# Kernel tuning notes

Measured on AMD Instinct MI355X. Metric: run time of the kernel, lower is better.

## Reference

```python
import jax, jax.numpy as jnp
import numpy as np


def setup_inputs() -> dict:
    key = jax.random.key(0)
    ks = jax.random.split(key, 5)
    T, B, C, H, K = 2048, 8, 1024, 16, 7
    s = 1.0 / np.sqrt(C)
    return {
        "x": jax.random.normal(ks[0], (T, B, C), dtype=jnp.float32),
        "w_weight": jax.random.normal(ks[1], (H * K, C), dtype=jnp.float32) * s,
        "glu_w": jax.random.normal(ks[2], (2 * H, C), dtype=jnp.float32) * s,
        "glu_b": jnp.zeros((2 * H,), dtype=jnp.float32),
        "out_w": jax.random.normal(ks[3], (C, C), dtype=jnp.float32) * s,
        "out_b": jnp.zeros((C,), dtype=jnp.float32),
        "padding_l": 6,
    }


def reference(x, w_weight, glu_w, glu_b, out_w, out_b, padding_l):
    # x: (T, B, C) in TBC format
    T, B, C = x.shape
    H = glu_w.shape[0] // 2
    K = w_weight.shape[0] // H
    R = C // H  # channels per head

    # GLU gate: C -> 2H, split last dim, a * sigmoid(b)  -> (T, B, H)
    g = (x @ glu_w.T + glu_b).reshape(T, B, H, 2)
    gate = g[..., 0] * jax.nn.sigmoid(g[..., 1])

    # per-position per-head kernel weights, softmax over K -> (T, B, H, K)
    w = jax.nn.softmax((x @ w_weight.T).reshape(T, B, H, K), axis=-1)

    # depthwise dynamic conv: out[t] = sum_k w[t,k] * x_pad[t + k]
    xh = x.reshape(T, B, H, R)
    xp = jnp.pad(xh, ((padding_l, K - 1 - padding_l), (0, 0), (0, 0), (0, 0)))
    conv = jnp.zeros_like(xh)
    for k in range(K):  # K is small & static; avoids (B,H,T,K,R) unfold blowup
        conv = conv + w[..., k:k + 1] * jax.lax.dynamic_slice_in_dim(xp, k, T, axis=0)

    # gate per head, merge heads, output projection
    out = (conv * gate[..., None]).reshape(T, B, C)
    return out @ out_w.T + out_b
```

## Files before the change

### kernel.cpp

```cpp
#include <hip/hip_runtime.h>
#include <hip/hip_bf16.h>
#include <stdint.h>

#define T_DIM 2048
#define B_DIM 8
#define C_DIM 1024
#define H_DIM 16
#define K_DIM 7
#define M_DIM (T_DIM * B_DIM)
#define NLOG 144
#define CW_STRIDE 128

typedef __attribute__((ext_vector_type(8))) short short8;
typedef __attribute__((ext_vector_type(4))) float floatx4;

__device__ __forceinline__ ushort f2bf(float f) {
    __hip_bfloat16 h = __float2bfloat16(f);
    return *(ushort*)&h;
}

#define S_W  ((size_t)112 * C_DIM)
#define S_G  ((size_t)32 * C_DIM)
#define S_O  ((size_t)C_DIM * C_DIM)
#define S_WG (S_W + S_G)
#define S_CVT (S_WG + S_O)

__global__ __launch_bounds__(256) void cvt_w_kernel(
    const float* __restrict__ w_weight, const float* __restrict__ glu_w,
    const float* __restrict__ out_w,
    ushort* __restrict__ wb, ushort* __restrict__ Wb)
{
    size_t gid = ((size_t)blockIdx.x * 256 + threadIdx.x) * 4;
    const float* src; ushort* dst; size_t off;
    if (gid < S_W)            { src = w_weight; dst = wb;       off = gid; }
    else if (gid < S_WG)      { src = glu_w;    dst = wb + S_W; off = gid - S_W; }
    else                      { src = out_w;    dst = Wb;       off = gid - S_WG; }
    float4 v = *(const float4*)(src + off);
    ushort4 o; o.x = f2bf(v.x); o.y = f2bf(v.y); o.z = f2bf(v.z); o.w = f2bf(v.w);
    *(ushort4*)(dst + off) = o;
}

__global__ __launch_bounds__(256) void logits_kernel(
    const float* __restrict__ x,
    const ushort* __restrict__ wb,
    const float* __restrict__ glu_b,
    float* __restrict__ cw)
{
    __shared__ __align__(16) ushort Bs[2][144 * 32];
    __shared__ float lsm[64][NLOG];

    const int tid = threadIdx.x;
    const int wave = tid >> 6, lane = tid & 63;
    const int fr = lane & 15, q = lane >> 4;
    const int m0 = blockIdx.x * 64;
    const int mrow = m0 + wave * 16 + fr;

    floatx4 acc[9];
#pragma unroll
    for (int j = 0; j < 9; ++j) acc[j] = (floatx4){0.f, 0.f, 0.f, 0.f};

    const float* arow = x + (size_t)mrow * C_DIM + q * 8;

    for (int i = tid; i < 576; i += 256) {
        int r = i >> 2, ch = i & 3;
        __builtin_amdgcn_global_load_lds(
            (const __attribute__((address_space(1))) void*)(wb + (size_t)r * C_DIM + ch * 8),
            (__attribute__((address_space(3))) void*)(&Bs[0][0] + i * 8), 16, 0, 0);
    }
    float4 a0 = *(const float4*)(arow);
    float4 a1 = *(const float4*)(arow + 4);
    __syncthreads();

    for (int kc = 0; kc < 32; ++kc) {
        const int buf = kc & 1;
        if (kc < 31) {
            const ushort* wsrc = wb + (kc + 1) * 32;
            for (int i = tid; i < 576; i += 256) {
                int r = i >> 2, ch = i & 3;
                __builtin_amdgcn_global_load_lds(
                    (const __attribute__((address_space(1))) void*)(wsrc + (size_t)r * C_DIM + ch * 8),
                    (__attribute__((address_space(3))) void*)(&Bs[buf ^ 1][0] + i * 8), 16, 0, 0);
            }
        }
        short8 a;
        a[0] = (short)f2bf(a0.x); a[1] = (short)f2bf(a0.y);
        a[2] = (short)f2bf(a0.z); a[3] = (short)f2bf(a0.w);
        a[4] = (short)f2bf(a1.x); a[5] = (short)f2bf(a1.y);
        a[6] = (short)f2bf(a1.z); a[7] = (short)f2bf(a1.w);
        if (kc < 31) {
            a0 = *(const float4*)(arow + (kc + 1) * 32);
            a1 = *(const float4*)(arow + (kc + 1) * 32 + 4);
        }
#pragma unroll
        for (int j = 0; j < 9; ++j) {
            short8 b = *(const short8*)(&Bs[buf][0] + ((j * 16 + fr) * 4 + q) * 8);
            acc[j] = __builtin_amdgcn_mfma_f32_16x16x32_bf16(a, b, acc[j], 0, 0, 0);
        }
        __syncthreads();
    }

#pragma unroll
    for (int j = 0; j < 9; ++j)
#pragma unroll
        for (int r = 0; r < 4; ++r)
            lsm[wave * 16 + q * 4 + r][j * 16 + fr] = acc[j][r];
    __syncthreads();

    {
        const int row = tid >> 2;
        const int hbase = (tid & 3) * 4;
        float* crow = cw + (size_t)(m0 + row) * CW_STRIDE;
#pragma unroll
        for (int hh = 0; hh < 4; ++hh) {
            const int h = hbase + hh;
            float l[K_DIM];
            float mx = -1e30f;
#pragma unroll
            for (int k = 0; k < K_DIM; ++k) { l[k] = lsm[row][h * K_DIM + k]; mx = fmaxf(mx, l[k]); }
            float s = 0.f;
#pragma unroll
            for (int k = 0; k < K_DIM; ++k) { l[k] = __expf(l[k] - mx); s += l[k]; }
            float inv = 1.f / s;
#pragma unroll
            for (int k = 0; k < K_DIM; ++k) crow[h * K_DIM + k] = l[k] * inv;
            float ga = lsm[row][112 + 2 * h] + glu_b[2 * h];
            float gb = lsm[row][113 + 2 * h] + glu_b[2 * h + 1];
            crow[112 + h] = ga * (1.f / (1.f + __expf(-gb)));
        }
    }
}

__global__ __launch_bounds__(256) void conv_kernel(
    const float* __restrict__ x,
    const float* __restrict__ cw,
    const int* __restrict__ padding_l_,
    ushort* __restrict__ y)
{
    const int lb = (blockIdx.x & 7) * 512 + (blockIdx.x >> 3);
    const int wave = threadIdx.x >> 6, lane = threadIdx.x & 63;
    const int m = lb * 4 + wave;
    const int t = m >> 3;
    const int pad = *padding_l_;
    const int h = lane >> 2;

    const float* crow = cw + (size_t)m * CW_STRIDE;
    float wt[K_DIM];
#pragma unroll
    for (int k = 0; k < K_DIM; ++k) wt[k] = crow[h * K_DIM + k];
    const float g = crow[112 + h];

    const int c0 = lane * 16;
    float av[16];
#pragma unroll
    for (int i = 0; i < 16; ++i) av[i] = 0.f;

#pragma unroll
    for (int k = 0; k < K_DIM; ++k) {
        int ts = t + k - pad;
        if (ts < 0 || ts >= T_DIM) continue;
        float wv = wt[k];
        const float4* xp = (const float4*)(x + ((size_t)m + 8 * (k - pad)) * C_DIM + c0);
        float4 u0 = xp[0], u1 = xp[1], u2 = xp[2], u3 = xp[3];
        av[0]  += wv * u0.x; av[1]  += wv * u0.y; av[2]  += wv * u0.z; av[3]  += wv * u0.w;
        av[4]  += wv * u1.x; av[5]  += wv * u1.y; av[6]  += wv * u1.z; av[7]  += wv * u1.w;
        av[8]  += wv * u2.x; av[9]  += wv * u2.y; av[10] += wv * u2.z; av[11] += wv * u2.w;
        av[12] += wv * u3.x; av[13] += wv * u3.y; av[14] += wv * u3.z; av[15] += wv * u3.w;
    }

    uint32_t o[8];
#pragma unroll
    for (int i = 0; i < 8; ++i)
        o[i] = (uint32_t)f2bf(av[2 * i] * g) | ((uint32_t)f2bf(av[2 * i + 1] * g) << 16);
    uint4* yr = (uint4*)(y + (size_t)m * C_DIM + c0);
    yr[0] = (uint4){o[0], o[1], o[2], o[3]};
    yr[1] = (uint4){o[4], o[5], o[6], o[7]};
}

__global__ __launch_bounds__(256) void out_gemm(
    const ushort* __restrict__ y,
    const ushort* __restrict__ Wb,
    const float* __restrict__ bias,
    float* __restrict__ out)
{
    __shared__ __align__(16) ushort As[128 * 64];
    __shared__ __align__(16) ushort Bs[128 * 64];

    const int bn = blockIdx.x & 7;
    const int bm = blockIdx.x >> 3;
    const int m0 = bm * 128, n0 = bn * 128;
    const int tid = threadIdx.x;
    const int lane = tid & 63, wave = tid >> 6;
    const int wm = (wave >> 1) * 64, wn = (wave & 1) * 64;
    const int fr = lane & 15, q = lane >> 4;

    floatx4 acc[4][4];
#pragma unroll
    for (int i = 0; i < 4; ++i)
#pragma unroll
        for (int j = 0; j < 4; ++j) acc[i][j] = (floatx4){0.f, 0.f, 0.f, 0.f};

    for (int k0 = 0; k0 < C_DIM; k0 += 64) {
        __syncthreads();
#pragma unroll
        for (int j = 0; j < 4; ++j) {
            int idx = j * 256 + tid;
            int r = idx >> 3, cl = idx & 7;
            int ch = cl ^ (r & 7);
            const ushort* ga = y + (size_t)(m0 + r) * C_DIM + k0 + ch * 8;
            __builtin_amdgcn_global_load_lds(
                (const __attribute__((address_space(1))) void*)ga,
                (__attribute__((address_space(3))) void*)(As + idx * 8), 16, 0, 0);
            const ushort* gb = Wb + (size_t)(n0 + r) * C_DIM + k0 + ch * 8;
            __builtin_amdgcn_global_load_lds(
                (const __attribute__((address_space(1))) void*)gb,
                (__attribute__((address_space(3))) void*)(Bs + idx * 8), 16, 0, 0);
        }
        __syncthreads();

#pragma unroll
        for (int s = 0; s < 64; s += 32) {
            const int cbase = (s >> 3) + q;
            short8 a[4], b[4];
#pragma unroll
            for (int i = 0; i < 4; ++i) {
                int r = wm + i * 16 + fr;
                a[i] = *(const short8*)(As + r * 64 + ((cbase ^ (r & 7)) * 8));
            }
#pragma unroll
            for (int j = 0; j < 4; ++j) {
                int r = wn + j * 16 + fr;
                b[j] = *(const short8*)(Bs + r * 64 + ((cbase ^ (r & 7)) * 8));
            }
#pragma unroll
            for (int i = 0; i < 4; ++i)
#pragma unroll
                for (int j = 0; j < 4; ++j)
                    acc[i][j] = __builtin_amdgcn_mfma_f32_16x16x32_bf16(a[i], b[j], acc[i][j], 0, 0, 0);
        }
    }

#pragma unroll
    for (int j = 0; j < 4; ++j) {
        int n = n0 + wn + j * 16 + fr;
        float bv = bias[n];
#pragma unroll
        for (int i = 0; i < 4; ++i) {
#pragma unroll
            for (int r = 0; r < 4; ++r) {
                int m = m0 + wm + i * 16 + q * 4 + r;
                out[(size_t)m * C_DIM + n] = acc[i][j][r] + bv;
            }
        }
    }
}

extern "C" void kernel_launch(void* const* d_in, const int* in_sizes, int n_in,
                              void* d_out, int out_size, void* d_ws, size_t ws_size,
                              hipStream_t stream) {
    const float* x        = (const float*)d_in[0];
    const float* w_weight = (const float*)d_in[1];
    const float* glu_w    = (const float*)d_in[2];
    const float* glu_b    = (const float*)d_in[3];
    const float* out_w    = (const float*)d_in[4];
    const float* out_b    = (const float*)d_in[5];
    const int* padding_l  = (const int*)d_in[6];
    float* out = (float*)d_out;

    char* ws = (char*)d_ws;
    ushort* y  = (ushort*)ws;
    ushort* wb = y + (size_t)M_DIM * C_DIM;
    ushort* Wb = wb + S_WG;
    float* cwp = (float*)(Wb + S_O);

    cvt_w_kernel<<<S_CVT / 4 / 256, 256, 0, stream>>>(w_weight, glu_w, out_w, wb, Wb);
    logits_kernel<<<M_DIM / 64, 256, 0, stream>>>(x, wb, glu_b, cwp);
    conv_kernel<<<M_DIM / 4, 256, 0, stream>>>(x, cwp, padding_l, y);
    out_gemm<<<(M_DIM / 128) * (C_DIM / 128), 256, 0, stream>>>(y, Wb, out_b, out);
}
```

Before: 229.7 us.

## Double-buffer out_gemm LDS tiles and stage epilogue through LDS for coalesced stores

Turns the out_gemm main loop into a two-stage LDS pipeline: the next K-tile is prefetched with global_load_lds while the current tile feeds the MFMAs, synchronised with manual vmcnt waits and barriers. The epilogue also writes the accumulators to LDS, then each thread adds bias to a float4 and stores it with a nontemporal vector store, replacing scattered scalar stores. This doubles LDS use (64KB), which may lower occupancy, and depends on the hand-written waitcnt counts being correct.

```diff
diff --git a/kernel.cpp b/kernel.cpp
--- a/kernel.cpp
+++ b/kernel.cpp
@@ -182,8 +182,7 @@
     const float* __restrict__ bias,
     float* __restrict__ out)
 {
-    __shared__ __align__(16) ushort As[128 * 64];
-    __shared__ __align__(16) ushort Bs[128 * 64];
+    __shared__ __align__(16) ushort SM[2][2][128 * 64];
 
     const int bn = blockIdx.x & 7;
     const int bm = blockIdx.x >> 3;
@@ -199,24 +198,37 @@
 #pragma unroll
         for (int j = 0; j < 4; ++j) acc[i][j] = (floatx4){0.f, 0.f, 0.f, 0.f};
 
-    for (int k0 = 0; k0 < C_DIM; k0 += 64) {
-        __syncthreads();
+    auto stage = [&](int buf, int k0) {
 #pragma unroll
         for (int j = 0; j < 4; ++j) {
             int idx = j * 256 + tid;
             int r = idx >> 3, cl = idx & 7;
             int ch = cl ^ (r & 7);
-            const ushort* ga = y + (size_t)(m0 + r) * C_DIM + k0 + ch * 8;
             __builtin_amdgcn_global_load_lds(
-                (const __attribute__((address_space(1))) void*)ga,
-                (__attribute__((address_space(3))) void*)(As + idx * 8), 16, 0, 0);
-            const ushort* gb = Wb + (size_t)(n0 + r) * C_DIM + k0 + ch * 8;
+                (const __attribute__((address_space(1))) void*)(y + (size_t)(m0 + r) * C_DIM + k0 + ch * 8),
+                (__attribute__((address_space(3))) void*)(&SM[buf][0][0] + idx * 8), 16, 0, 0);
             __builtin_amdgcn_global_load_lds(
-                (const __attribute__((address_space(1))) void*)gb,
-                (__attribute__((address_space(3))) void*)(Bs + idx * 8), 16, 0, 0);
-        }
-        __syncthreads();
-
+                (const __attribute__((address_space(1))) void*)(Wb + (size_t)(n0 + r) * C_DIM + k0 + ch * 8),
+                (__attribute__((address_space(3))) void*)(&SM[buf][1][0] + idx * 8), 16, 0, 0);
+        }
+    };
+
+    stage(0, 0);
+
+#pragma unroll 2
+    for (int kt = 0; kt < 16; ++kt) {
+        const int buf = kt & 1;
+        if (kt < 15) {
+            stage(buf ^ 1, (kt + 1) * 64);
+            asm volatile("s_waitcnt vmcnt(8)" ::: "memory");
+        } else {
+            asm volatile("s_waitcnt vmcnt(0)" ::: "memory");
+        }
+        __builtin_amdgcn_s_barrier();
+        asm volatile("" ::: "memory");
+
+        const ushort* Ab = &SM[buf][0][0];
+        const ushort* Bb = &SM[buf][1][0];
 #pragma unroll
         for (int s = 0; s < 64; s += 32) {
             const int cbase = (s >> 3) + q;
@@ -224,12 +236,12 @@
 #pragma unroll
             for (int i = 0; i < 4; ++i) {
                 int r = wm + i * 16 + fr;
-                a[i] = *(const short8*)(As + r * 64 + ((cbase ^ (r & 7)) * 8));
+                a[i] = *(const short8*)(Ab + r * 64 + ((cbase ^ (r & 7)) * 8));
             }
 #pragma unroll
             for (int j = 0; j < 4; ++j) {
                 int r = wn + j * 16 + fr;
-                b[j] = *(const short8*)(Bs + r * 64 + ((cbase ^ (r & 7)) * 8));
+                b[j] = *(const short8*)(Bb + r * 64 + ((cbase ^ (r & 7)) * 8));
             }
 #pragma unroll
             for (int i = 0; i < 4; ++i)
@@ -237,19 +249,31 @@
                 for (int j = 0; j < 4; ++j)
                     acc[i][j] = __builtin_amdgcn_mfma_f32_16x16x32_bf16(a[i], b[j], acc[i][j], 0, 0, 0);
         }
-    }
-
-#pragma unroll
-    for (int j = 0; j < 4; ++j) {
-        int n = n0 + wn + j * 16 + fr;
-        float bv = bias[n];
-#pragma unroll
-        for (int i = 0; i < 4; ++i) {
-#pragma unroll
-            for (int r = 0; r < 4; ++r) {
-                int m = m0 + wm + i * 16 + q * 4 + r;
-                out[(size_t)m * C_DIM + n] = acc[i][j][r] + bv;
-            }
+
+        asm volatile("" ::: "memory");
+        __builtin_amdgcn_s_barrier();
+        asm volatile("" ::: "memory");
+    }
+
+    float* Cs = (float*)&SM[0][0][0];
+#pragma unroll
+    for (int i = 0; i < 4; ++i)
+#pragma unroll
+        for (int j = 0; j < 4; ++j)
+#pragma unroll
+            for (int r = 0; r < 4; ++r)
+                Cs[(wm + i * 16 + q * 4 + r) * 128 + (wn + j * 16 + fr)] = acc[i][j][r];
+    __syncthreads();
+
+    {
+        const int c4 = (tid & 31) * 4;
+        floatx4 bv = *(const floatx4*)(bias + n0 + c4);
+#pragma unroll
+        for (int rep = 0; rep < 16; ++rep) {
+            int row = rep * 8 + (tid >> 5);
+            floatx4 v = *(const floatx4*)(Cs + row * 128 + c4);
+            v = v + bv;
+            __builtin_nontemporal_store(v, (floatx4*)(out + (size_t)(m0 + row) * C_DIM + n0 + c4));
         }
     }
 }
```

Measured after the change: 234.1 us. No clear change (+1.9%).
